# Kernel tuning notes

Measured on AMD Instinct MI355X. Metric: run time of the kernel, lower is better.

## Reference

```python
import jax, jax.numpy as jnp
import numpy as np

B, S, D = 1, 2048, 2048
NH, NKV, HD = 32, 8, 64
D_FIBER, D_CONTROL = 16, 64
ALPHA = 0.995  # ema_momentum
NEG = -1e9


def setup_inputs() -> dict:
    key = jax.random.key(0)
    ks = jax.random.split(key, 10)
    hidden_states = jax.random.normal(ks[0], (B, S, D), dtype=jnp.float32)
    # causal additive mask [1,1,S,S]
    causal = jnp.tril(jnp.ones((S, S), dtype=bool))
    attention_mask = jnp.where(causal, 0.0, NEG).astype(jnp.float32)[None, None]
    # RoPE tables [S, HD]
    inv_freq = 1.0 / (10000.0 ** (np.arange(0, HD, 2, dtype=np.float32) / HD))
    pos = np.arange(S, dtype=np.float32)
    freqs = pos[:, None] * inv_freq[None, :]
    emb = np.concatenate([freqs, freqs], axis=-1)
    cos = jnp.asarray(np.cos(emb), dtype=jnp.float32)
    sin = jnp.asarray(np.sin(emb), dtype=jnp.float32)
    # adapter params
    Wf = 0.02 * jax.random.normal(ks[1], (D, D_FIBER), dtype=jnp.float32)
    W1 = jax.random.normal(ks[2], (D + D_FIBER, D_CONTROL), dtype=jnp.float32) * (2.0 / (D + D_FIBER + D_CONTROL)) ** 0.5
    b1 = jnp.zeros((D_CONTROL,), dtype=jnp.float32)
    W2 = jax.random.normal(ks[3], (D_CONTROL, 1), dtype=jnp.float32) * (2.0 / (D_CONTROL + 1)) ** 0.5
    b2 = 0.1 * jax.random.normal(ks[4], (1,), dtype=jnp.float32)
    gate_scale = jnp.float32(0.5)
    # attention projections (Llama-style, no bias); stored as [in, out]
    s = 1.0 / np.sqrt(D)
    Wq = s * jax.random.normal(ks[5], (D, NH * HD), dtype=jnp.float32)
    Wk = s * jax.random.normal(ks[6], (D, NKV * HD), dtype=jnp.float32)
    Wv = s * jax.random.normal(ks[7], (D, NKV * HD), dtype=jnp.float32)
    Wo = s * jax.random.normal(ks[8], (NH * HD, D), dtype=jnp.float32)
    return dict(hidden_states=hidden_states, attention_mask=attention_mask,
                cos=cos, sin=sin, Wf=Wf, W1=W1, b1=b1, W2=W2, b2=b2,
                gate_scale=gate_scale, Wq=Wq, Wk=Wk, Wv=Wv, Wo=Wo)


def _rotate_half(x):
    x1, x2 = jnp.split(x, 2, axis=-1)
    return jnp.concatenate([-x2, x1], axis=-1)


def reference(hidden_states, attention_mask, cos, sin, Wf, W1, b1, W2, b2,
              gate_scale, Wq, Wk, Wv, Wo):
    h = hidden_states.astype(jnp.float32)  # [B,S,D]
    # ---- CFAdapter ----
    fiber = h @ Wf                                      # [B,S,d_fiber]
    combined = jnp.concatenate([h, fiber], axis=-1)     # [B,S,D+d_fiber]
    hmid = jax.nn.gelu(combined @ W1 + b1, approximate=False)
    risk = (hmid @ W2 + b2)[..., 0]                     # [B,S]
    field = (1.0 - ALPHA) * risk                        # prev_field is None
    f_mean = field.mean(axis=1, keepdims=True)
    f_std = field.std(axis=1, keepdims=True, ddof=1) + 1e-6  # torch unbiased std
    gate = (field - f_mean) / f_std                     # [B,S]
    # ---- attention with inline RoPE + gate bias ----
    q = (h @ Wq).reshape(B, S, NH, HD).transpose(0, 2, 1, 3)   # [B,NH,S,HD]
    k = (h @ Wk).reshape(B, S, NKV, HD).transpose(0, 2, 1, 3)  # [B,NKV,S,HD]
    v = (h @ Wv).reshape(B, S, NKV, HD).transpose(0, 2, 1, 3)
    q = q * cos + _rotate_half(q) * sin
    k = k * cos + _rotate_half(k) * sin
    n_rep = NH // NKV
    k = jnp.repeat(k, n_rep, axis=1)  # repeat_interleave semantics
    v = jnp.repeat(v, n_rep, axis=1)
    scores = jnp.einsum('bhqd,bhkd->bhqk', q, k) / jnp.sqrt(jnp.float32(HD))
    scores = scores + attention_mask + gate_scale * gate[:, None, None, :]
    attn = jax.nn.softmax(scores.astype(jnp.float32), axis=-1).astype(q.dtype)
    out = jnp.einsum('bhqk,bhkd->bhqd', attn, v)
    out = out.transpose(0, 2, 1, 3).reshape(B, S, NH * HD)
    out = out @ Wo
    return out
```

## Files before the change

kernel.cpp:

```cpp
#include <hip/hip_runtime.h>

#define S_LEN 2048
#define D_DIM 2048
#define NHEAD 32
#define NKVH  8
#define HDIM  64
#define NBT   3200

typedef __attribute__((ext_vector_type(4))) float f32x4;
typedef __attribute__((ext_vector_type(8))) short bf16x8;

__device__ __forceinline__ unsigned short f2bf(float x) {
    union { float f; unsigned u; } v; v.f = x;
    unsigned r = v.u + 0x7FFFu + ((v.u >> 16) & 1u);
    return (unsigned short)(r >> 16);
}

#define GLD(gsrc, ldst) __builtin_amdgcn_global_load_lds( \
    (const __attribute__((address_space(1))) unsigned int*)(const void*)(gsrc), \
    (__attribute__((address_space(3))) unsigned int*)(void*)(ldst), 16, 0, 0)

#define SWZ(r) (((r) & 7) << 4)

#define KPERM(kk) (((kk) & 32) | (((kk) & 12) << 1) | (((kk) & 16) >> 2) | ((kk) & 3))

__device__ __forceinline__ void dev_trans(const float* __restrict__ W, unsigned short* __restrict__ WT,
                                          int N, int k0, int n0, int t, unsigned short L[64][65]) {
    for (int it = 0; it < 16; ++it) {
        int e = it * 256 + t;
        int r = e >> 6, c = e & 63;
        L[c][r] = f2bf(W[(size_t)(k0 + r) * N + n0 + c]);
    }
    __syncthreads();
    for (int it = 0; it < 16; ++it) {
        int e = it * 256 + t;
        int n = e >> 6, kk = e & 63;
        WT[(size_t)(n0 + n) * 2048 + k0 + kk] = L[n][kk];
    }
}

__global__ __launch_bounds__(256) void k_prep(const float* __restrict__ h, unsigned short* __restrict__ hb,
        const float* __restrict__ Wq, const float* __restrict__ Wk, const float* __restrict__ Wv,
        const float* __restrict__ Wo, const float* __restrict__ Wf, const float* __restrict__ W1,
        unsigned short* __restrict__ bt, unsigned short* __restrict__ wot) {
    __shared__ unsigned short L[64][65];
    int b = blockIdx.x, t = threadIdx.x;
    if (b < 4096) {
        int i = (b * 256 + t) * 4;
        float4 v = *(const float4*)(h + i);
        ushort4 o;
        o.x = f2bf(v.x); o.y = f2bf(v.y); o.z = f2bf(v.z); o.w = f2bf(v.w);
        *(ushort4*)(hb + i) = o;
    } else if (b < 5120) {
        int bb = b - 4096;
        dev_trans(Wq, bt, 2048, (bb & 31) * 64, (bb >> 5) * 64, t, L);
    } else if (b < 5376) {
        int bb = b - 5120;
        dev_trans(Wk, bt + (size_t)2048 * 2048, 512, (bb & 31) * 64, (bb >> 5) * 64, t, L);
    } else if (b < 5632) {
        int bb = b - 5376;
        dev_trans(Wv, bt + (size_t)2560 * 2048, 512, (bb & 31) * 64, (bb >> 5) * 64, t, L);
    } else if (b < 6656) {
        int bb = b - 5632;
        dev_trans(Wo, wot, 2048, (bb & 31) * 64, (bb >> 5) * 64, t, L);
    } else if (b < 6688) {
        int k0 = (b - 6656) * 64;
        for (int it = 0; it < 4; ++it) {
            int e = it * 256 + t;
            int r = e >> 4, c = e & 15;
            L[c][r] = f2bf(Wf[(size_t)(k0 + r) * 16 + c]);
        }
        __syncthreads();
        unsigned short* dst = bt + (size_t)3072 * 2048;
        for (int it = 0; it < 4; ++it) {
            int e = it * 256 + t;
            int c = e >> 6, kk = e & 63;
            dst[(size_t)c * 2048 + k0 + kk] = L[c][kk];
        }
    } else if (b < 6720) {
        int k0 = (b - 6688) * 64;
        dev_trans(W1, bt + (size_t)3088 * 2048, 64, k0, 0, t, L);
    } else {
        int bb = b - 6720;
        unsigned* p = (unsigned*)(bt + (size_t)3152 * 2048);
        p[bb * 256 + t] = 0u;
    }
}

__global__ __launch_bounds__(256) void k_fuse_vtrans(const float* __restrict__ adcols,
                        const float* __restrict__ W1, const float* __restrict__ b1,
                        const float* __restrict__ W2, const float* __restrict__ b2,
                        float* __restrict__ field,
                        const unsigned short* __restrict__ vrow, unsigned short* __restrict__ vt) {
    __shared__ unsigned short L[64][65];
    int b = blockIdx.x, t = threadIdx.x;
    if (b < 512) {
        int wv = t >> 6, l = t & 63;
        int s = b * 4 + wv;
        const float* row = adcols + (size_t)s * 128;
        float x = row[16 + l] + b1[l];
#pragma unroll
        for (int f = 0; f < 16; ++f) x += row[f] * W1[(size_t)(2048 + f) * 64 + l];
        float hm = 0.5f * x * (1.f + erff(x * 0.70710678118654752f));
        float p = hm * W2[l];
        for (int m = 32; m; m >>= 1) p += __shfl_xor(p, m);
        if (l == 0) field[s] = 0.005f * (p + b2[0]);
    } else {
        int bb = b - 512;
        int s0 = (bb & 31) * 64, hk = bb >> 5;
        for (int it = 0; it < 16; ++it) {
            int e = it * 256 + t;
            int r = e >> 6, c = e & 63;
            L[c][r] = vrow[(size_t)(s0 + r) * 512 + hk * 64 + c];
        }
        __syncthreads();
        for (int it = 0; it < 16; ++it) {
            int e = it * 256 + t;
            int c = e >> 6, kk = e & 63;
            vt[((size_t)hk * 64 + c) * S_LEN + s0 + KPERM(kk)] = L[c][kk];
        }
    }
}

__global__ void k_gate(const float* __restrict__ field, float* __restrict__ gate) {
    __shared__ float red[256];
    int t = threadIdx.x;
    float s = 0.f;
    for (int i = t; i < S_LEN; i += 256) s += field[i];
    red[t] = s; __syncthreads();
    for (int w = 128; w; w >>= 1) { if (t < w) red[t] += red[t + w]; __syncthreads(); }
    float mean = red[0] / (float)S_LEN;
    __syncthreads();
    float v = 0.f;
    for (int i = t; i < S_LEN; i += 256) { float d = field[i] - mean; v += d * d; }
    red[t] = v; __syncthreads();
    for (int w = 128; w; w >>= 1) { if (t < w) red[t] += red[t + w]; __syncthreads(); }
    float stdv = sqrtf(red[0] / (float)(S_LEN - 1)) + 1e-6f;
    for (int i = t; i < S_LEN; i += 256) gate[i] = (field[i] - mean) / stdv;
}

__global__ __launch_bounds__(256) void k_gemm_qkv(const unsigned short* __restrict__ A,
                                                  const unsigned short* __restrict__ BT,
                                                  const float* __restrict__ cs,
                                                  const float* __restrict__ sn,
                                                  unsigned short* __restrict__ qb,
                                                  unsigned short* __restrict__ kbuf,
                                                  unsigned short* __restrict__ vrow,
                                                  float* __restrict__ adcols) {
    __shared__ __align__(16) char As[4096];
    __shared__ __align__(16) char Bs[8192];
    const int K = 2048;
    int flat = blockIdx.y * gridDim.x + blockIdx.x;
    int cpx = (gridDim.x * gridDim.y) >> 3;
    int swz = (flat & 7) * cpx + (flat >> 3);
    int m0 = (swz / gridDim.x) * 64, n0 = (swz % gridDim.x) * 128;
    int t = threadIdx.x;
    int wv = t >> 6, ln = t & 63;
    int wr = (wv >> 1) * 32, wc = (wv & 1) * 64;
    int lr = ln & 15, lkb = (ln >> 4) * 16;
    f32x4 acc[2][4] = {};
    const unsigned short* Ap = A + (size_t)(m0 + (t >> 2)) * K + (t & 3) * 8;
    const unsigned short* Bp = BT + (size_t)(n0 + (t >> 2)) * K + (t & 3) * 8;
    char* lA = As + wv * 1024;
    char* lB = Bs + wv * 1024;
    int nk = K / 32;
    GLD(Ap, lA);
    GLD(Bp, lB); GLD(Bp + (size_t)64 * K, lB + 4096);
    for (int kt = 0; kt < nk; ++kt) {
        __syncthreads();
        bf16x8 af[2], bfv[4];
#pragma unroll
        for (int i = 0; i < 2; ++i) af[i]  = *(const bf16x8*)(As + (wr + i * 16 + lr) * 64 + lkb);
#pragma unroll
        for (int j = 0; j < 4; ++j) bfv[j] = *(const bf16x8*)(Bs + (wc + j * 16 + lr) * 64 + lkb);
#pragma unroll
        for (int i = 0; i < 2; ++i)
#pragma unroll
            for (int j = 0; j < 4; ++j)
                acc[i][j] = __builtin_amdgcn_mfma_f32_16x16x32_bf16(af[i], bfv[j], acc[i][j], 0, 0, 0);
        __syncthreads();
        if (kt + 1 < nk) {
            const unsigned short* Ak = Ap + (size_t)(kt + 1) * 32;
            const unsigned short* Bk = Bp + (size_t)(kt + 1) * 32;
            GLD(Ak, lA);
            GLD(Bk, lB); GLD(Bk + (size_t)64 * K, lB + 4096);
        }
    }
    int orow = (ln >> 4) * 4;
    int col0 = n0 + wc;
    if (col0 < 2560) {
        bool isq = (col0 < 2048);
        unsigned short* dst = isq ? qb : kbuf;
        int hh = (isq ? col0 : col0 - 2048) >> 6;
        float qscale = isq ? 0.125f : 1.0f;
#pragma unroll
        for (int i = 0; i < 2; ++i)
#pragma unroll
            for (int r = 0; r < 4; ++r) {
                int s = m0 + wr + i * 16 + orow + r;
#pragma unroll
                for (int j = 0; j < 4; ++j) {
                    int d = j * 16 + lr;
                    float c = cs[s * 64 + d], si = sn[s * 64 + d];
                    float val = acc[i][j][r];
                    float prt = acc[i][j ^ 2][r];
                    float out = val * c + ((j < 2) ? -prt : prt) * si;
                    dst[((size_t)hh * S_LEN + s) * 64 + d] = f2bf(out * qscale);
                }
            }
    } else if (col0 < 3072) {
        int vc0 = col0 - 2560;
#pragma unroll
        for (int i = 0; i < 2; ++i)
#pragma unroll
            for (int j = 0; j < 4; ++j) {
                unsigned short* vp = vrow + (size_t)(m0 + wr + i * 16 + orow) * 512 + vc0 + j * 16 + lr;
                for (int r = 0; r < 4; ++r) vp[(size_t)r * 512] = f2bf(acc[i][j][r]);
            }
    } else {
        int ac0 = col0 - 3072;
#pragma unroll
        for (int i = 0; i < 2; ++i)
#pragma unroll
            for (int j = 0; j < 4; ++j) {
                float* ap = adcols + (size_t)(m0 + wr + i * 16 + orow) * 128 + ac0 + j * 16 + lr;
                for (int r = 0; r < 4; ++r) ap[(size_t)r * 128] = acc[i][j][r];
            }
    }
}

__global__ __launch_bounds__(256) void k_gemm(const unsigned short* __restrict__ A,
                                              const unsigned short* __restrict__ BT,
                                              float* __restrict__ C, int M, int N, int K) {
    __shared__ __align__(16) char As[4096];
    __shared__ __align__(16) char Bs[8192];
    int flat = blockIdx.y * gridDim.x + blockIdx.x;
    int cpx = (gridDim.x * gridDim.y) >> 3;
    int swz = (flat & 7) * cpx + (flat >> 3);
    int m0 = (swz / gridDim.x) * 64, n0 = (swz % gridDim.x) * 128;
    int t = threadIdx.x;
    int wv = t >> 6, ln = t & 63;
    int wr = (wv >> 1) * 32, wc = (wv & 1) * 64;
    int lr = ln & 15, lkb = (ln >> 4) * 16;
    f32x4 acc[2][4] = {};
    const unsigned short* Ap = A + (size_t)(m0 + (t >> 2)) * K + (t & 3) * 8;
    const unsigned short* Bp = BT + (size_t)(n0 + (t >> 2)) * K + (t & 3) * 8;
    char* lA = As + wv * 1024;
    char* lB = Bs + wv * 1024;
    int nk = K / 32;
    GLD(Ap, lA);
    GLD(Bp, lB); GLD(Bp + (size_t)64 * K, lB + 4096);
    for (int kt = 0; kt < nk; ++kt) {
        __syncthreads();
        bf16x8 af[2], bfv[4];
#pragma unroll
        for (int i = 0; i < 2; ++i) af[i]  = *(const bf16x8*)(As + (wr + i * 16 + lr) * 64 + lkb);
#pragma unroll
        for (int j = 0; j < 4; ++j) bfv[j] = *(const bf16x8*)(Bs + (wc + j * 16 + lr) * 64 + lkb);
#pragma unroll
        for (int i = 0; i < 2; ++i)
#pragma unroll
            for (int j = 0; j < 4; ++j)
                acc[i][j] = __builtin_amdgcn_mfma_f32_16x16x32_bf16(af[i], bfv[j], acc[i][j], 0, 0, 0);
        __syncthreads();
        if (kt + 1 < nk) {
            const unsigned short* Ak = Ap + (size_t)(kt + 1) * 32;
            const unsigned short* Bk = Bp + (size_t)(kt + 1) * 32;
            GLD(Ak, lA);
            GLD(Bk, lB); GLD(Bk + (size_t)64 * K, lB + 4096);
        }
    }
    int orow = (ln >> 4) * 4;
#pragma unroll
    for (int i = 0; i < 2; ++i)
#pragma unroll
        for (int j = 0; j < 4; ++j) {
            float* Cp = C + (size_t)(m0 + wr + i * 16 + orow) * N + n0 + wc + j * 16 + lr;
            for (int r = 0; r < 4; ++r) Cp[(size_t)r * N] = acc[i][j][r];
        }
}

__device__ __forceinline__ bf16x8 packP(const f32x4& a, const f32x4& b) {
    union { unsigned u[4]; bf16x8 v; } pk;
    asm("v_cvt_pk_bf16_f32 %0, %1, %2" : "=v"(pk.u[0]) : "v"(a[0]), "v"(a[1]));
    asm("v_cvt_pk_bf16_f32 %0, %1, %2" : "=v"(pk.u[1]) : "v"(a[2]), "v"(a[3]));
    asm("v_cvt_pk_bf16_f32 %0, %1, %2" : "=v"(pk.u[2]) : "v"(b[0]), "v"(b[1]));
    asm("v_cvt_pk_bf16_f32 %0, %1, %2" : "=v"(pk.u[3]) : "v"(b[2]), "v"(b[3]));
    return pk.v;
}

__global__ __launch_bounds__(128, 2) void k_attn(const unsigned short* __restrict__ qb,
                                                 const unsigned short* __restrict__ kb,
                                                 const unsigned short* __restrict__ vt,
                                                 const float* __restrict__ gate,
                                                 const float* __restrict__ gs_p,
                                                 unsigned short* __restrict__ attnout) {
    __shared__ __align__(16) char Kl[2][8192];
    __shared__ __align__(16) char Vl[2][8192];
    int h = blockIdx.y, hk = h >> 2;
    int qt = (h < 16) ? (31 - blockIdx.x) : blockIdx.x;
    int t = threadIdx.x, wv = t >> 6, l = t & 63;
    int lq = l & 15, lg = l >> 4;
    float gs = gs_p[0];
    int q0 = qt * 64 + wv * 32;
    const unsigned short* qbase = qb + ((size_t)h * S_LEN + q0) * 64;
    bf16x8 aq[2][2];
#pragma unroll
    for (int qf = 0; qf < 2; ++qf)
#pragma unroll
        for (int hf = 0; hf < 2; ++hf)
            aq[qf][hf] = *(const bf16x8*)(qbase + (qf * 16 + lq) * 64 + hf * 32 + lg * 8);
    f32x4 o[2][4] = {};
    float m_[2] = { -INFINITY, -INFINITY };
    float ls_[2] = { 0.f, 0.f };
    int nkt = qt + 1;
    int srow = t >> 3;
    int scol = 8 * ((t & 7) ^ (srow & 7));
    const unsigned short* kg = kb + (size_t)hk * S_LEN * 64;
    const unsigned short* vg = vt + (size_t)hk * 64 * S_LEN;
    char* lKb0 = Kl[0] + wv * 1024; char* lKb1 = Kl[1] + wv * 1024;
    char* lVb0 = Vl[0] + wv * 1024; char* lVb1 = Vl[1] + wv * 1024;
#define STAGE_KV(K0, DK, DV) do { \
        GLD(kg + (size_t)((K0) + srow) * 64 + scol, (DK)); \
        GLD(kg + (size_t)((K0) + 16 + srow) * 64 + scol, (DK) + 2048); \
        GLD(kg + (size_t)((K0) + 32 + srow) * 64 + scol, (DK) + 4096); \
        GLD(kg + (size_t)((K0) + 48 + srow) * 64 + scol, (DK) + 6144); \
        GLD(vg + (size_t)srow * S_LEN + (K0) + scol, (DV)); \
        GLD(vg + (size_t)(16 + srow) * S_LEN + (K0) + scol, (DV) + 2048); \
        GLD(vg + (size_t)(32 + srow) * S_LEN + (K0) + scol, (DV) + 4096); \
        GLD(vg + (size_t)(48 + srow) * S_LEN + (K0) + scol, (DV) + 6144); \
    } while (0)
    STAGE_KV(0, lKb0, lVb0);
    for (int kt = 0; kt < nkt; ++kt) {
        __syncthreads();
        if (kt + 1 < nkt) {
            int k0n = (kt + 1) * 64;
            char* dK = ((kt + 1) & 1) ? lKb1 : lKb0;
            char* dV = ((kt + 1) & 1) ? lVb1 : lVb0;
            STAGE_KV(k0n, dK, dV);
        }
        int k0 = kt * 64;
        bool diag = (kt == nkt - 1);
        const char* Kb = Kl[kt & 1];
        const char* Vb = Vl[kt & 1];
        f32x4 sc[2][4] = {};
#pragma unroll
        for (int ct = 0; ct < 4; ++ct) {
            int krow = ct * 16 + lq;
#pragma unroll
            for (int hf = 0; hf < 2; ++hf) {
                bf16x8 bk = *(const bf16x8*)(Kb + krow * 128 + ((hf * 64 + lg * 16) ^ SWZ(krow)));
#pragma unroll
                for (int qf = 0; qf < 2; ++qf)
                    sc[qf][ct] = __builtin_amdgcn_mfma_f32_16x16x32_bf16(bk, aq[qf][hf], sc[qf][ct], 0, 0, 0);
            }
        }
        float vmax[2] = { -INFINITY, -INFINITY };
#pragma unroll
        for (int ct = 0; ct < 4; ++ct) {
            f32x4 g4 = *(const f32x4*)(gate + k0 + ct * 16 + lg * 4);
#pragma unroll
            for (int qf = 0; qf < 2; ++qf) {
                int q = q0 + qf * 16 + lq;
#pragma unroll
                for (int r = 0; r < 4; ++r) {
                    float val = sc[qf][ct][r] + gs * g4[r];
                    if (diag && (k0 + ct * 16 + lg * 4 + r > q)) val = -1e9f;
                    sc[qf][ct][r] = val;
                    vmax[qf] = fmaxf(vmax[qf], val);
                }
            }
        }
#pragma unroll
        for (int qf = 0; qf < 2; ++qf) {
            vmax[qf] = fmaxf(vmax[qf], __shfl_xor(vmax[qf], 16));
            vmax[qf] = fmaxf(vmax[qf], __shfl_xor(vmax[qf], 32));
        }
        bool cond = (vmax[0] <= m_[0] + 8.f) && (vmax[1] <= m_[1] + 8.f);
        if (!__all(cond)) {
#pragma unroll
            for (int qf = 0; qf < 2; ++qf) {
                float mn = fmaxf(m_[qf], vmax[qf]);
                float scl = __expf(m_[qf] - mn);
                ls_[qf] *= scl;
#pragma unroll
                for (int dt = 0; dt < 4; ++dt) o[qf][dt] *= scl;
                m_[qf] = mn;
            }
        }
#pragma unroll
        for (int qf = 0; qf < 2; ++qf)
#pragma unroll
            for (int ct = 0; ct < 4; ++ct)
#pragma unroll
                for (int r = 0; r < 4; ++r) {
                    float p = __expf(sc[qf][ct][r] - m_[qf]);
                    sc[qf][ct][r] = p;
                    ls_[qf] += p;
                }
#pragma unroll
        for (int ks = 0; ks < 2; ++ks) {
            bf16x8 pf0 = packP(sc[0][2 * ks], sc[0][2 * ks + 1]);
            bf16x8 pf1 = packP(sc[1][2 * ks], sc[1][2 * ks + 1]);
#pragma unroll
            for (int dt = 0; dt < 4; ++dt) {
                int vr = dt * 16 + lq;
                bf16x8 bv = *(const bf16x8*)(Vb + vr * 128 + ((ks * 64 + lg * 16) ^ SWZ(vr)));
                o[0][dt] = __builtin_amdgcn_mfma_f32_16x16x32_bf16(bv, pf0, o[0][dt], 0, 0, 0);
                o[1][dt] = __builtin_amdgcn_mfma_f32_16x16x32_bf16(bv, pf1, o[1][dt], 0, 0, 0);
            }
        }
    }
#undef STAGE_KV
#pragma unroll
    for (int qf = 0; qf < 2; ++qf) {
        float s = ls_[qf];
        s += __shfl_xor(s, 16);
        s += __shfl_xor(s, 32);
        float inv = 1.f / s;
        int q = q0 + qf * 16 + lq;
        unsigned short* orow = attnout + (size_t)q * 2048 + h * 64;
#pragma unroll
        for (int dt = 0; dt < 4; ++dt) {
            ushort4 st;
            st.x = f2bf(o[qf][dt][0] * inv); st.y = f2bf(o[qf][dt][1] * inv);
            st.z = f2bf(o[qf][dt][2] * inv); st.w = f2bf(o[qf][dt][3] * inv);
            *(ushort4*)(orow + dt * 16 + lg * 4) = st;
        }
    }
}

extern "C" void kernel_launch(void* const* d_in, const int* in_sizes, int n_in,
                              void* d_out, int out_size, void* d_ws, size_t ws_size,
                              hipStream_t stream) {
    const float* h    = (const float*)d_in[0];
    const float* cosT = (const float*)d_in[2];
    const float* sinT = (const float*)d_in[3];
    const float* Wf   = (const float*)d_in[4];
    const float* W1   = (const float*)d_in[5];
    const float* b1   = (const float*)d_in[6];
    const float* W2   = (const float*)d_in[7];
    const float* b2   = (const float*)d_in[8];
    const float* gs   = (const float*)d_in[9];
    const float* Wq   = (const float*)d_in[10];
    const float* Wk   = (const float*)d_in[11];
    const float* Wv   = (const float*)d_in[12];
    const float* Wo   = (const float*)d_in[13];
    float* out = (float*)d_out;

    char* ws = (char*)d_ws;
    unsigned short* hb     = (unsigned short*)(ws);
    unsigned short* bt     = (unsigned short*)(ws + 8388608);
    unsigned short* qbuf   = (unsigned short*)(ws + 21495808);
    unsigned short* kbuf   = (unsigned short*)(ws + 29884416);
    unsigned short* vrow   = (unsigned short*)(ws + 31981568);
    float*          adcols = (float*)(ws + 34078720);
    float*          field  = (float*)(ws + 35127296);
    float*          gate   = (float*)(ws + 35135488);
    unsigned short* wot    = (unsigned short*)(ws + 35143680);
    unsigned short* vt      = (unsigned short*)(ws + 16777216);
    unsigned short* attnout = (unsigned short*)(ws);

    k_prep<<<dim3(6912), dim3(256), 0, stream>>>(h, hb, Wq, Wk, Wv, Wo, Wf, W1, bt, wot);
    k_gemm_qkv<<<dim3(25, 32), dim3(256), 0, stream>>>(hb, bt, cosT, sinT, qbuf, kbuf, vrow, adcols);
    k_fuse_vtrans<<<dim3(768), dim3(256), 0, stream>>>(adcols, W1, b1, W2, b2, field, vrow, vt);
    k_gate<<<dim3(1), dim3(256), 0, stream>>>(field, gate);
    k_attn<<<dim3(32, 32), dim3(128), 0, stream>>>(qbuf, kbuf, vt, gate, gs, attnout);
    k_gemm<<<dim3(16, 32), dim3(256), 0, stream>>>(attnout, wot, out, 2048, 2048, 2048);
}
```

Measured before the change: 168.0 us.

## Double GEMM K-tile to 64 with XOR-swizzled LDS layout

Both GEMM kernels now share a gemm_core helper that stages K=64 slices per iteration instead of K=32. This halves the number of barrier pairs and load rounds per tile. LDS rows are now 128 bytes, with an XOR swizzle on the global-load column to avoid bank conflicts on the fragment reads. The cost is twice the shared memory per block, which may lower occupancy, and the loads within an iteration are still not overlapped with compute.

```diff
diff --git a/kernel.cpp b/kernel.cpp
--- a/kernel.cpp
+++ b/kernel.cpp
@@ -139,6 +139,59 @@
     for (int i = t; i < S_LEN; i += 256) gate[i] = (field[i] - mean) / stdv;
 }
 
+__device__ __forceinline__ void gemm_core(const unsigned short* __restrict__ A,
+                                          const unsigned short* __restrict__ BT,
+                                          int K, int m0, int n0,
+                                          char* As, char* Bs,
+                                          int wr, int wc, int lr, int lkb,
+                                          f32x4 acc[2][4]) {
+    int t = threadIdx.x;
+    int wv = t >> 6;
+    int srow = t >> 3;
+    int scol = 8 * ((t & 7) ^ (srow & 7));
+    const unsigned short* Ag = A + (size_t)(m0 + srow) * K + scol;
+    const unsigned short* Bg = BT + (size_t)(n0 + srow) * K + scol;
+    char* lA = As + wv * 1024;
+    char* lB = Bs + wv * 1024;
+    int nk = K / 64;
+    GLD(Ag, lA); GLD(Ag + (size_t)32 * K, lA + 4096);
+    GLD(Bg, lB); GLD(Bg + (size_t)32 * K, lB + 4096);
+    GLD(Bg + (size_t)64 * K, lB + 8192); GLD(Bg + (size_t)96 * K, lB + 12288);
+    for (int kt = 0; kt < nk; ++kt) {
+        __syncthreads();
+        bf16x8 af[2][2], bfv[4][2];
+#pragma unroll
+        for (int i = 0; i < 2; ++i) {
+            int row = wr + i * 16 + lr;
+#pragma unroll
+            for (int kh = 0; kh < 2; ++kh)
+                af[i][kh] = *(const bf16x8*)(As + row * 128 + ((kh * 64 + lkb) ^ SWZ(row)));
+        }
+#pragma unroll
+        for (int j = 0; j < 4; ++j) {
+            int row = wc + j * 16 + lr;
+#pragma unroll
+            for (int kh = 0; kh < 2; ++kh)
+                bfv[j][kh] = *(const bf16x8*)(Bs + row * 128 + ((kh * 64 + lkb) ^ SWZ(row)));
+        }
+#pragma unroll
+        for (int kh = 0; kh < 2; ++kh)
+#pragma unroll
+            for (int i = 0; i < 2; ++i)
+#pragma unroll
+                for (int j = 0; j < 4; ++j)
+                    acc[i][j] = __builtin_amdgcn_mfma_f32_16x16x32_bf16(af[i][kh], bfv[j][kh], acc[i][j], 0, 0, 0);
+        __syncthreads();
+        if (kt + 1 < nk) {
+            const unsigned short* Ak = Ag + (size_t)(kt + 1) * 64;
+            const unsigned short* Bk = Bg + (size_t)(kt + 1) * 64;
+            GLD(Ak, lA); GLD(Ak + (size_t)32 * K, lA + 4096);
+            GLD(Bk, lB); GLD(Bk + (size_t)32 * K, lB + 4096);
+            GLD(Bk + (size_t)64 * K, lB + 8192); GLD(Bk + (size_t)96 * K, lB + 12288);
+        }
+    }
+}
+
 __global__ __launch_bounds__(256) void k_gemm_qkv(const unsigned short* __restrict__ A,
                                                   const unsigned short* __restrict__ BT,
                                                   const float* __restrict__ cs,
@@ -147,8 +200,8 @@
                                                   unsigned short* __restrict__ kbuf,
                                                   unsigned short* __restrict__ vrow,
                                                   float* __restrict__ adcols) {
-    __shared__ __align__(16) char As[4096];
-    __shared__ __align__(16) char Bs[8192];
+    __shared__ __align__(16) char As[8192];
+    __shared__ __align__(16) char Bs[16384];
     const int K = 2048;
     int flat = blockIdx.y * gridDim.x + blockIdx.x;
     int cpx = (gridDim.x * gridDim.y) >> 3;
@@ -159,33 +212,7 @@
     int wr = (wv >> 1) * 32, wc = (wv & 1) * 64;
     int lr = ln & 15, lkb = (ln >> 4) * 16;
     f32x4 acc[2][4] = {};
-    const unsigned short* Ap = A + (size_t)(m0 + (t >> 2)) * K + (t & 3) * 8;
-    const unsigned short* Bp = BT + (size_t)(n0 + (t >> 2)) * K + (t & 3) * 8;
-    char* lA = As + wv * 1024;
-    char* lB = Bs + wv * 1024;
-    int nk = K / 32;
-    GLD(Ap, lA);
-    GLD(Bp, lB); GLD(Bp + (size_t)64 * K, lB + 4096);
-    for (int kt = 0; kt < nk; ++kt) {
-        __syncthreads();
-        bf16x8 af[2], bfv[4];
-#pragma unroll
-        for (int i = 0; i < 2; ++i) af[i]  = *(const bf16x8*)(As + (wr + i * 16 + lr) * 64 + lkb);
-#pragma unroll
-        for (int j = 0; j < 4; ++j) bfv[j] = *(const bf16x8*)(Bs + (wc + j * 16 + lr) * 64 + lkb);
-#pragma unroll
-        for (int i = 0; i < 2; ++i)
-#pragma unroll
-            for (int j = 0; j < 4; ++j)
-                acc[i][j] = __builtin_amdgcn_mfma_f32_16x16x32_bf16(af[i], bfv[j], acc[i][j], 0, 0, 0);
-        __syncthreads();
-        if (kt + 1 < nk) {
-            const unsigned short* Ak = Ap + (size_t)(kt + 1) * 32;
-            const unsigned short* Bk = Bp + (size_t)(kt + 1) * 32;
-            GLD(Ak, lA);
-            GLD(Bk, lB); GLD(Bk + (size_t)64 * K, lB + 4096);
-        }
-    }
+    gemm_core(A, BT, K, m0, n0, As, Bs, wr, wc, lr, lkb, acc);
     int orow = (ln >> 4) * 4;
     int col0 = n0 + wc;
     if (col0 < 2560) {
@@ -232,8 +259,8 @@
 __global__ __launch_bounds__(256) void k_gemm(const unsigned short* __restrict__ A,
                                               const unsigned short* __restrict__ BT,
                                               float* __restrict__ C, int M, int N, int K) {
-    __shared__ __align__(16) char As[4096];
-    __shared__ __align__(16) char Bs[8192];
+    __shared__ __align__(16) char As[8192];
+    __shared__ __align__(16) char Bs[16384];
     int flat = blockIdx.y * gridDim.x + blockIdx.x;
     int cpx = (gridDim.x * gridDim.y) >> 3;
     int swz = (flat & 7) * cpx + (flat >> 3);
@@ -243,33 +270,7 @@
     int wr = (wv >> 1) * 32, wc = (wv & 1) * 64;
     int lr = ln & 15, lkb = (ln >> 4) * 16;
     f32x4 acc[2][4] = {};
-    const unsigned short* Ap = A + (size_t)(m0 + (t >> 2)) * K + (t & 3) * 8;
-    const unsigned short* Bp = BT + (size_t)(n0 + (t >> 2)) * K + (t & 3) * 8;
-    char* lA = As + wv * 1024;
-    char* lB = Bs + wv * 1024;
-    int nk = K / 32;
-    GLD(Ap, lA);
-    GLD(Bp, lB); GLD(Bp + (size_t)64 * K, lB + 4096);
-    for (int kt = 0; kt < nk; ++kt) {
-        __syncthreads();
-        bf16x8 af[2], bfv[4];
-#pragma unroll
-        for (int i = 0; i < 2; ++i) af[i]  = *(const bf16x8*)(As + (wr + i * 16 + lr) * 64 + lkb);
-#pragma unroll
-        for (int j = 0; j < 4; ++j) bfv[j] = *(const bf16x8*)(Bs + (wc + j * 16 + lr) * 64 + lkb);
-#pragma unroll
-        for (int i = 0; i < 2; ++i)
-#pragma unroll
-            for (int j = 0; j < 4; ++j)
-                acc[i][j] = __builtin_amdgcn_mfma_f32_16x16x32_bf16(af[i], bfv[j], acc[i][j], 0, 0, 0);
-        __syncthreads();
-        if (kt + 1 < nk) {
-            const unsigned short* Ak = Ap + (size_t)(kt + 1) * 32;
-            const unsigned short* Bk = Bp + (size_t)(kt + 1) * 32;
-            GLD(Ak, lA);
-            GLD(Bk, lB); GLD(Bk + (size_t)64 * K, lB + 4096);
-        }
-    }
+    gemm_core(A, BT, K, m0, n0, As, Bs, wr, wc, lr, lkb, acc);
     int orow = (ln >> 4) * 4;
 #pragma unroll
     for (int i = 0; i < 2; ++i)
```

Result: faster. 156.2 us (median of 3 runs) (-7.0%).
